# Kernel tuning notes

Hardware: AMD Instinct MI355X
Metric: run time of the kernel (lower is better)

Reference implementation:

```python
import jax, jax.numpy as jnp
import numpy as np

DIM = 768
NUM_HEADS = 16
HEAD_DIM = DIM // NUM_HEADS
SCALE = HEAD_DIM ** -0.5


def setup_inputs() -> dict:
    key = jax.random.key(0)
    ks = jax.random.split(key, 5)
    B, S = 2, 2048
    x = jax.random.normal(ks[0], (B, S, DIM), dtype=jnp.float32)
    # nn.Linear(dim, dim, bias=False): weight shape [out, in]; y = x @ W.T
    init = 1.0 / np.sqrt(DIM)
    Wq = jax.random.uniform(ks[1], (DIM, DIM), jnp.float32, -init, init)
    Wk = jax.random.uniform(ks[2], (DIM, DIM), jnp.float32, -init, init)
    Wv = jax.random.uniform(ks[3], (DIM, DIM), jnp.float32, -init, init)
    Wo = jax.random.uniform(ks[4], (DIM, DIM), jnp.float32, -init, init)
    return {"x": x, "Wq": Wq, "Wk": Wk, "Wv": Wv, "Wo": Wo}


def reference(x, Wq, Wk, Wv, Wo):
    B, S, _ = x.shape
    # projections (torch Linear: x @ W.T)
    q = jnp.einsum('bsd,ed->bse', x, Wq).reshape(B, S, NUM_HEADS, HEAD_DIM)
    k = jnp.einsum('bsd,ed->bse', x, Wk).reshape(B, S, NUM_HEADS, HEAD_DIM)
    v = jnp.einsum('bsd,ed->bse', x, Wv).reshape(B, S, NUM_HEADS, HEAD_DIM)
    # [B, H, S, S] scores, stable softmax, then context
    scores = jnp.einsum('bqhd,bkhd->bhqk', q, k) * SCALE
    probs = jax.nn.softmax(scores, axis=-1)  # dropout is identity in eval
    ctx = jnp.einsum('bhqk,bkhd->bqhd', probs, v).reshape(B, S, DIM)
    return jnp.einsum('bsd,ed->bse', ctx, Wo)
```

## Files before the change

### kernel.cpp

```cpp
#include <hip/hip_runtime.h>
#include <cstdint>

#define DIM 768
#define SEQ 2048
#define NB 2
#define NH 16
#define HD 48
#define NROWS (NB*SEQ)

typedef __attribute__((ext_vector_type(8))) short bf16x8;
typedef __attribute__((ext_vector_type(4))) float f32x4;
typedef __attribute__((ext_vector_type(16))) float f32x16;
typedef unsigned int u32;

__device__ __forceinline__ short f2bf(float f) {
    union { float f; uint32_t u; } v; v.f = f;
    uint32_t u = v.u;
    uint32_t r = (u + 0x7FFFu + ((u >> 16) & 1u)) >> 16;
    return (short)r;
}

__device__ __forceinline__ u32 cvtpk(float lo, float hi) {
    u32 r;
    asm("v_cvt_pk_bf16_f32 %0, %1, %2" : "=v"(r) : "v"(lo), "v"(hi));
    return r;
}
__device__ __forceinline__ bf16x8 pack8(float4 a, float4 b) {
    int4 w = make_int4((int)cvtpk(a.x, a.y), (int)cvtpk(a.z, a.w),
                       (int)cvtpk(b.x, b.y), (int)cvtpk(b.z, b.w));
    return __builtin_bit_cast(bf16x8, w);
}

template<bool A_F32, bool OUT_F32>
__global__ __launch_bounds__(256)
void gemm96(const void* __restrict__ Av,
            const float* __restrict__ B0, const float* __restrict__ B1,
            const float* __restrict__ B2,
            void* __restrict__ C0v, void* __restrict__ C1v, void* __restrict__ C2v)
{
    const float* B = B0; void* Cv = C0v;
    if (blockIdx.z == 1) { B = B1; Cv = C1v; }
    else if (blockIdx.z == 2) { B = B2; Cv = C2v; }

    __shared__ short As[128*64];
    __shared__ short Bs[96*64];

    const int tid  = threadIdx.x;
    const int lane = tid & 63;
    const int wid  = tid >> 6;
    const int wr = wid >> 1, wc = wid & 1;
    const int m  = lane & 15, kb = lane >> 4;
    const int m0 = blockIdx.y * 128, n0 = blockIdx.x * 96;

    f32x4 acc[4][3];
#pragma unroll
    for (int i = 0; i < 4; ++i)
#pragma unroll
        for (int j = 0; j < 3; ++j) acc[i][j] = (f32x4){0.f,0.f,0.f,0.f};

    bf16x8 sa[4], sb[3];

#define LOAD_A(k0, i) {                                                       \
        int c = tid + (i)*256; int row = c >> 3, gs = (c & 7) ^ (row & 7);    \
        if (A_F32) {                                                          \
            const float* p = (const float*)Av + (size_t)(m0+row)*DIM + (k0) + gs*8; \
            sa[i] = pack8(*(const float4*)p, *(const float4*)(p+4));          \
        } else {                                                              \
            sa[i] = *(const bf16x8*)((const short*)Av + (size_t)(m0+row)*DIM + (k0) + gs*8); \
        } }
#define LOAD_B(k0, i) {                                                       \
        int c = tid + (i)*256; int row = c >> 3, gs = (c & 7) ^ (row & 7);    \
        const float* p = B + (size_t)(n0+row)*DIM + (k0) + gs*8;              \
        sb[i] = pack8(*(const float4*)p, *(const float4*)(p+4)); }

#pragma unroll
    for (int i = 0; i < 4; ++i) LOAD_A(0, i);
#pragma unroll
    for (int i = 0; i < 3; ++i) LOAD_B(0, i);

    for (int kt = 0; kt < DIM/64; ++kt) {
        __syncthreads();
#pragma unroll
        for (int i = 0; i < 4; ++i) {
            int c = tid + i*256;
            *(bf16x8*)&As[(c>>3)*64 + (c&7)*8] = sa[i];
        }
#pragma unroll
        for (int i = 0; i < 3; ++i) {
            int c = tid + i*256;
            *(bf16x8*)&Bs[(c>>3)*64 + (c&7)*8] = sb[i];
        }
        __syncthreads();

        if (kt < DIM/64 - 1) {
            int k0 = (kt+1)*64;
#pragma unroll
            for (int i = 0; i < 4; ++i) LOAD_A(k0, i);
#pragma unroll
            for (int i = 0; i < 3; ++i) LOAD_B(k0, i);
        }

        bf16x8 af[2][4], bfr[2][3];
#pragma unroll
        for (int t = 0; t < 2; ++t) {
            int sl = ((t*4 + kb) ^ (m & 7)) * 8;
#pragma unroll
            for (int f = 0; f < 4; ++f)
                af[t][f]  = *(const bf16x8*)&As[(wr*64 + f*16 + m)*64 + sl];
#pragma unroll
            for (int f = 0; f < 3; ++f)
                bfr[t][f] = *(const bf16x8*)&Bs[(wc*48 + f*16 + m)*64 + sl];
        }
#pragma unroll
        for (int fm = 0; fm < 4; ++fm)
#pragma unroll
            for (int fn = 0; fn < 3; ++fn) {
                acc[fm][fn] = __builtin_amdgcn_mfma_f32_16x16x32_bf16(af[0][fm], bfr[0][fn], acc[fm][fn], 0, 0, 0);
                acc[fm][fn] = __builtin_amdgcn_mfma_f32_16x16x32_bf16(af[1][fm], bfr[1][fn], acc[fm][fn], 0, 0, 0);
            }
    }
#undef LOAD_A
#undef LOAD_B

#pragma unroll
    for (int fm = 0; fm < 4; ++fm)
#pragma unroll
        for (int fn = 0; fn < 3; ++fn) {
            int col = n0 + wc*48 + fn*16 + m;
#pragma unroll
            for (int r = 0; r < 4; ++r) {
                int row = m0 + wr*64 + fm*16 + kb*4 + r;
                if (OUT_F32)
                    ((float*)Cv)[(size_t)row*DIM + col] = acc[fm][fn][r];
                else
                    ((short*)Cv)[(size_t)row*DIM + col] = f2bf(acc[fm][fn][r]);
            }
        }
}

__global__ __launch_bounds__(256)
void flash2(const short* __restrict__ Qb, const short* __restrict__ Kb,
            const short* __restrict__ Vb, short* __restrict__ Ctx)
{
    __shared__ short K_lds[64*64];
    __shared__ short Vt_lds[64*68];

    const int tid  = threadIdx.x;
    const int wid  = tid >> 6, lane = tid & 63;
    const int r    = lane & 31, hi = lane >> 5;
    const size_t base = (size_t)blockIdx.z*SEQ*DIM + (size_t)blockIdx.y*HD;
    const int q0 = blockIdx.x*128 + wid*32;
    const float C2  = 0.20823688f;
    const float THR = 11.5f;

    for (int i = tid; i < 16*68; i += 256) Vt_lds[48*68 + i] = 0;

    bf16x8 qf[3];
#pragma unroll
    for (int s = 0; s < 3; ++s)
        qf[s] = *(const bf16x8*)&Qb[base + (size_t)(q0 + r)*DIM + s*16 + hi*8];

    f32x16 z16;
#pragma unroll
    for (int i = 0; i < 16; ++i) z16[i] = 0.f;

    f32x16 acc0 = z16, acc1 = z16;
    float m_i = -1e30f, l_i = 0.f;

    const int row0 = tid >> 3,       ps0 = tid & 7;
    const int row1 = (tid+256) >> 3, ps1 = tid & 7;
    const int ls0 = ps0 ^ (row0 & 7), ls1 = ps1 ^ (row1 & 7);

    bf16x8 k0r, k1r; short vreg[12];
    k0r = *(const bf16x8*)&Kb[base + (size_t)row0*DIM + ls0*8];
    k1r = *(const bf16x8*)&Kb[base + (size_t)row1*DIM + ls1*8];
#pragma unroll
    for (int j = 0; j < 12; ++j)
        vreg[j] = Vb[base + (size_t)lane*DIM + wid*12 + j];

    for (int t = 0; t < SEQ/64; ++t) {
        __syncthreads();
        *(bf16x8*)&K_lds[row0*64 + ps0*8] = k0r;
        *(bf16x8*)&K_lds[row1*64 + ps1*8] = k1r;
#pragma unroll
        for (int j = 0; j < 12; ++j)
            Vt_lds[(wid*12 + j)*68 + lane] = vreg[j];
        __syncthreads();

        if (t + 1 < SEQ/64) {
            int c0 = (t+1)*64;
            k0r = *(const bf16x8*)&Kb[base + (size_t)(c0 + row0)*DIM + ls0*8];
            k1r = *(const bf16x8*)&Kb[base + (size_t)(c0 + row1)*DIM + ls1*8];
#pragma unroll
            for (int j = 0; j < 12; ++j)
                vreg[j] = Vb[base + (size_t)(c0 + lane)*DIM + wid*12 + j];
        }

        f32x16 sa[2];
#pragma unroll
        for (int ct = 0; ct < 2; ++ct) {
            f32x16 a = z16;
#pragma unroll
            for (int s = 0; s < 3; ++s) {
                int row = ct*32 + r;
                bf16x8 kf = *(const bf16x8*)&K_lds[row*64 + ((s*2+hi) ^ (row&7))*8];
                a = __builtin_amdgcn_mfma_f32_32x32x16_bf16(kf, qf[s], a, 0, 0, 0);
            }
            sa[ct] = a;
        }

        float mx = -1e30f;
#pragma unroll
        for (int ct = 0; ct < 2; ++ct)
#pragma unroll
            for (int i = 0; i < 16; ++i) mx = fmaxf(mx, sa[ct][i]);
        mx = fmaxf(mx, __shfl_xor(mx, 32));
        mx *= C2;

        float mn = m_i;
        if (!__all(mx - m_i <= THR)) {
            mn = fmaxf(m_i, mx);
            float al = exp2f(m_i - mn);
            l_i *= al;
#pragma unroll
            for (int i = 0; i < 16; ++i) { acc0[i] *= al; acc1[i] *= al; }
            m_i = mn;
        }

        float rs = 0.f;
        u32 w[2][8], sw[2][8];
#pragma unroll
        for (int ct = 0; ct < 2; ++ct)
#pragma unroll
            for (int k = 0; k < 8; ++k) {
                float p0 = exp2f(fmaf(sa[ct][2*k],   C2, -mn));
                float p1 = exp2f(fmaf(sa[ct][2*k+1], C2, -mn));
                w[ct][k] = cvtpk(p0, p1);
                rs += p0 + p1;
            }
        rs += __shfl_xor(rs, 32);
        l_i += rs;
#pragma unroll
        for (int ct = 0; ct < 2; ++ct)
#pragma unroll
            for (int k = 0; k < 8; ++k) sw[ct][k] = (u32)__shfl_xor((int)w[ct][k], 32);

#pragma unroll
        for (int ct = 0; ct < 2; ++ct)
#pragma unroll
            for (int hf = 0; hf < 2; ++hf) {
                u32 f0 = hi ? sw[ct][4*hf+2] : w[ct][4*hf+0];
                u32 f1 = hi ? sw[ct][4*hf+3] : w[ct][4*hf+1];
                u32 f2 = hi ? w[ct][4*hf+2]  : sw[ct][4*hf+0];
                u32 f3 = hi ? w[ct][4*hf+3]  : sw[ct][4*hf+1];
                int4 pw = make_int4((int)f0, (int)f1, (int)f2, (int)f3);
                bf16x8 pb = __builtin_bit_cast(bf16x8, pw);
#pragma unroll
                for (int dt = 0; dt < 2; ++dt) {
                    int off = (dt*32 + r)*68 + ct*32 + hf*16 + hi*8;
                    short4 v0 = *(const short4*)&Vt_lds[off];
                    short4 v1 = *(const short4*)&Vt_lds[off + 4];
                    bf16x8 av = {v0.x, v0.y, v0.z, v0.w, v1.x, v1.y, v1.z, v1.w};
                    if (dt == 0) acc0 = __builtin_amdgcn_mfma_f32_32x32x16_bf16(av, pb, acc0, 0, 0, 0);
                    else         acc1 = __builtin_amdgcn_mfma_f32_32x32x16_bf16(av, pb, acc1, 0, 0, 0);
                }
            }
    }

    float inv = 1.0f / l_i;
#pragma unroll
    for (int g = 0; g < 16; ++g) {
        int d = (g&3) + 8*(g>>2) + 4*hi;
        Ctx[base + (size_t)(q0 + r)*DIM + d] = f2bf(acc0[g] * inv);
    }
#pragma unroll
    for (int g = 0; g < 8; ++g) {
        int d = 32 + (g&3) + 8*(g>>2) + 4*hi;
        Ctx[base + (size_t)(q0 + r)*DIM + d] = f2bf(acc1[g] * inv);
    }
}

extern "C" void kernel_launch(void* const* d_in, const int* in_sizes, int n_in,
                              void* d_out, int out_size, void* d_ws, size_t ws_size,
                              hipStream_t stream)
{
    const float* x  = (const float*)d_in[0];
    const float* Wq = (const float*)d_in[1];
    const float* Wk = (const float*)d_in[2];
    const float* Wv = (const float*)d_in[3];
    const float* Wo = (const float*)d_in[4];
    float* out = (float*)d_out;

    const size_t XN = (size_t)NROWS * DIM;

    short* qb   = (short*)d_ws;
    short* kbuf = qb   + XN;
    short* vbuf = kbuf + XN;
    short* ctxb = vbuf + XN;

    dim3 g1(DIM/96, NROWS/128, 3);
    gemm96<true, false><<<g1, 256, 0, stream>>>(x, Wq, Wk, Wv, qb, kbuf, vbuf);

    dim3 g2(SEQ/128, NH, NB);
    flash2<<<g2, 256, 0, stream>>>(qb, kbuf, vbuf, ctxb);

    dim3 g3(DIM/96, NROWS/128, 1);
    gemm96<false, true><<<g3, 256, 0, stream>>>(ctxb, Wo, Wo, Wo, out, out, out);
}
```

Baseline: 196.5 us.

## Double-buffer K/V LDS tiles in flash attention with 128-thread blocks

Rewrites the attention kernel to use two LDS buffers for K and transposed V. The next tile is written into the idle buffer after compute, so each iteration needs one barrier instead of two. Blocks shrink to two waves (64 queries) and the grid doubles, giving more blocks per CU. V is now loaded with 16-byte vector loads instead of scalar shorts, and the row max uses three-input max trees. The cost is double the LDS per block and each block re-reading K/V for fewer queries, which increases global traffic.

```diff
diff --git a/kernel.cpp b/kernel.cpp
--- a/kernel.cpp
+++ b/kernel.cpp
@@ -30,6 +30,8 @@
                        (int)cvtpk(b.x, b.y), (int)cvtpk(b.z, b.w));
     return __builtin_bit_cast(bf16x8, w);
 }
+
+#define MAX3(a,b,c) fmaxf(fmaxf((a),(b)),(c))
 
 template<bool A_F32, bool OUT_F32>
 __global__ __launch_bounds__(256)
@@ -138,22 +140,25 @@
         }
 }
 
-__global__ __launch_bounds__(256)
-void flash2(const short* __restrict__ Qb, const short* __restrict__ Kb,
+__global__ __launch_bounds__(128)
+void flash3(const short* __restrict__ Qb, const short* __restrict__ Kb,
             const short* __restrict__ Vb, short* __restrict__ Ctx)
 {
-    __shared__ short K_lds[64*64];
-    __shared__ short Vt_lds[64*68];
+    __shared__ short K_lds[2][64*64];
+    __shared__ short Vt_lds[2][64*68];
 
     const int tid  = threadIdx.x;
     const int wid  = tid >> 6, lane = tid & 63;
     const int r    = lane & 31, hi = lane >> 5;
     const size_t base = (size_t)blockIdx.z*SEQ*DIM + (size_t)blockIdx.y*HD;
-    const int q0 = blockIdx.x*128 + wid*32;
+    const int q0 = blockIdx.x*64 + wid*32;
     const float C2  = 0.20823688f;
     const float THR = 11.5f;
 
-    for (int i = tid; i < 16*68; i += 256) Vt_lds[48*68 + i] = 0;
+    for (int i = tid; i < 2*16*68; i += 128) {
+        int bb = i / (16*68), rr = i - bb*(16*68);
+        Vt_lds[bb][48*68 + rr] = 0;
+    }
 
     bf16x8 qf[3];
 #pragma unroll
@@ -167,33 +172,47 @@
     f32x16 acc0 = z16, acc1 = z16;
     float m_i = -1e30f, l_i = 0.f;
 
-    const int row0 = tid >> 3,       ps0 = tid & 7;
-    const int row1 = (tid+256) >> 3, ps1 = tid & 7;
-    const int ls0 = ps0 ^ (row0 & 7), ls1 = ps1 ^ (row1 & 7);
-
-    bf16x8 k0r, k1r; short vreg[12];
-    k0r = *(const bf16x8*)&Kb[base + (size_t)row0*DIM + ls0*8];
-    k1r = *(const bf16x8*)&Kb[base + (size_t)row1*DIM + ls1*8];
-#pragma unroll
-    for (int j = 0; j < 12; ++j)
-        vreg[j] = Vb[base + (size_t)lane*DIM + wid*12 + j];
+    int krow[4], kps[4];
+#pragma unroll
+    for (int i = 0; i < 4; ++i) {
+        int c = tid + i*128;
+        krow[i] = c >> 3; kps[i] = c & 7;
+    }
+    const int vrow = tid & 63, vd0 = (tid >> 6) * 24;
+
+    bf16x8 kreg[4], vreg[3];
+#pragma unroll
+    for (int i = 0; i < 4; ++i) {
+        int ls = kps[i] ^ (krow[i] & 7);
+        kreg[i] = *(const bf16x8*)&Kb[base + (size_t)krow[i]*DIM + ls*8];
+    }
+#pragma unroll
+    for (int j = 0; j < 3; ++j)
+        vreg[j] = *(const bf16x8*)&Vb[base + (size_t)vrow*DIM + vd0 + j*8];
+
+#pragma unroll
+    for (int i = 0; i < 4; ++i)
+        *(bf16x8*)&K_lds[0][krow[i]*64 + kps[i]*8] = kreg[i];
+#pragma unroll
+    for (int j = 0; j < 3; ++j)
+#pragma unroll
+        for (int e = 0; e < 8; ++e)
+            Vt_lds[0][(vd0 + j*8 + e)*68 + vrow] = vreg[j][e];
 
     for (int t = 0; t < SEQ/64; ++t) {
-        __syncthreads();
-        *(bf16x8*)&K_lds[row0*64 + ps0*8] = k0r;
-        *(bf16x8*)&K_lds[row1*64 + ps1*8] = k1r;
-#pragma unroll
-        for (int j = 0; j < 12; ++j)
-            Vt_lds[(wid*12 + j)*68 + lane] = vreg[j];
+        const int cur = t & 1;
         __syncthreads();
 
         if (t + 1 < SEQ/64) {
             int c0 = (t+1)*64;
-            k0r = *(const bf16x8*)&Kb[base + (size_t)(c0 + row0)*DIM + ls0*8];
-            k1r = *(const bf16x8*)&Kb[base + (size_t)(c0 + row1)*DIM + ls1*8];
-#pragma unroll
-            for (int j = 0; j < 12; ++j)
-                vreg[j] = Vb[base + (size_t)(c0 + lane)*DIM + wid*12 + j];
+#pragma unroll
+            for (int i = 0; i < 4; ++i) {
+                int ls = kps[i] ^ (krow[i] & 7);
+                kreg[i] = *(const bf16x8*)&Kb[base + (size_t)(c0 + krow[i])*DIM + ls*8];
+            }
+#pragma unroll
+            for (int j = 0; j < 3; ++j)
+                vreg[j] = *(const bf16x8*)&Vb[base + (size_t)(c0 + vrow)*DIM + vd0 + j*8];
         }
 
         f32x16 sa[2];
@@ -203,7 +222,7 @@
 #pragma unroll
             for (int s = 0; s < 3; ++s) {
                 int row = ct*32 + r;
-                bf16x8 kf = *(const bf16x8*)&K_lds[row*64 + ((s*2+hi) ^ (row&7))*8];
+                bf16x8 kf = *(const bf16x8*)&K_lds[cur][row*64 + ((s*2+hi) ^ (row&7))*8];
                 a = __builtin_amdgcn_mfma_f32_32x32x16_bf16(kf, qf[s], a, 0, 0, 0);
             }
             sa[ct] = a;
@@ -211,9 +230,16 @@
 
         float mx = -1e30f;
 #pragma unroll
-        for (int ct = 0; ct < 2; ++ct)
-#pragma unroll
-            for (int i = 0; i < 16; ++i) mx = fmaxf(mx, sa[ct][i]);
+        for (int ct = 0; ct < 2; ++ct) {
+            float a = MAX3(sa[ct][0],  sa[ct][1],  sa[ct][2]);
+            float b = MAX3(sa[ct][3],  sa[ct][4],  sa[ct][5]);
+            float c = MAX3(sa[ct][6],  sa[ct][7],  sa[ct][8]);
+            float d = MAX3(sa[ct][9],  sa[ct][10], sa[ct][11]);
+            float e = MAX3(sa[ct][12], sa[ct][13], sa[ct][14]);
+            float f = MAX3(a, b, sa[ct][15]);
+            float g = MAX3(c, d, e);
+            mx = MAX3(mx, f, g);
+        }
         mx = fmaxf(mx, __shfl_xor(mx, 32));
         mx *= C2;
 
@@ -258,13 +284,25 @@
 #pragma unroll
                 for (int dt = 0; dt < 2; ++dt) {
                     int off = (dt*32 + r)*68 + ct*32 + hf*16 + hi*8;
-                    short4 v0 = *(const short4*)&Vt_lds[off];
-                    short4 v1 = *(const short4*)&Vt_lds[off + 4];
+                    short4 v0 = *(const short4*)&Vt_lds[cur][off];
+                    short4 v1 = *(const short4*)&Vt_lds[cur][off + 4];
                     bf16x8 av = {v0.x, v0.y, v0.z, v0.w, v1.x, v1.y, v1.z, v1.w};
                     if (dt == 0) acc0 = __builtin_amdgcn_mfma_f32_32x32x16_bf16(av, pb, acc0, 0, 0, 0);
                     else         acc1 = __builtin_amdgcn_mfma_f32_32x32x16_bf16(av, pb, acc1, 0, 0, 0);
                 }
             }
+
+        if (t + 1 < SEQ/64) {
+            const int nxt = cur ^ 1;
+#pragma unroll
+            for (int i = 0; i < 4; ++i)
+                *(bf16x8*)&K_lds[nxt][krow[i]*64 + kps[i]*8] = kreg[i];
+#pragma unroll
+            for (int j = 0; j < 3; ++j)
+#pragma unroll
+                for (int e = 0; e < 8; ++e)
+                    Vt_lds[nxt][(vd0 + j*8 + e)*68 + vrow] = vreg[j][e];
+        }
     }
 
     float inv = 1.0f / l_i;
@@ -301,8 +339,8 @@
     dim3 g1(DIM/96, NROWS/128, 3);
     gemm96<true, false><<<g1, 256, 0, stream>>>(x, Wq, Wk, Wv, qb, kbuf, vbuf);
 
-    dim3 g2(SEQ/128, NH, NB);
-    flash2<<<g2, 256, 0, stream>>>(qb, kbuf, vbuf, ctxb);
+    dim3 g2(SEQ/64, NH, NB);
+    flash3<<<g2, 128, 0, stream>>>(qb, kbuf, vbuf, ctxb);
 
     dim3 g3(DIM/96, NROWS/128, 1);
     gemm96<false, true><<<g3, 256, 0, stream>>>(ctxb, Wo, Wo, Wo, out, out, out);
```

Result: slower. 203.2 us (+3.4%).
